# Optimization experiments

Measured on AMD Instinct MI355X. Metric: run time of the kernel, lower is better.

The kernel has to match this reference:

```python
import jax, jax.numpy as jnp
import numpy as np

N = 100000
E = 3200000
IN_F = 256
OUT_F = 64
ALPHA = 0.2  # LeakyReLU negative slope


def setup_inputs() -> dict:
    key = jax.random.key(0)
    k1, k2, k3, k4 = jax.random.split(key, 4)
    adj = jax.random.randint(k1, (2, E), 0, N, dtype=jnp.int64)
    x = jax.random.normal(k2, (N, IN_F), dtype=jnp.float32)
    # xavier-normal-ish scales
    W_fc = jax.random.normal(k3, (OUT_F, IN_F), dtype=jnp.float32) * (1.414 * np.sqrt(2.0 / (IN_F + OUT_F)))
    b_fc = jnp.zeros((OUT_F,), dtype=jnp.float32)
    a = jax.random.normal(k4, (1, 2 * OUT_F), dtype=jnp.float32) * (1.414 * np.sqrt(2.0 / (1 + 2 * OUT_F)))
    return {"adj": adj, "x": x, "W_fc": W_fc, "b_fc": b_fc, "a": a}


def reference(adj, x, W_fc, b_fc, a):
    src = adj[0]  # [E]
    dst = adj[1]  # [E]
    h = x @ W_fc.T + b_fc                       # [N, OUT_F]
    a1, a2 = a[0, :OUT_F], a[0, OUT_F:]         # split of attention vector
    # e = leakyrelu(a . [h_src || h_dst]) computed without materializing concat
    s1 = h @ a1                                  # [N]
    s2 = h @ a2                                  # [N]
    e = s1[src] + s2[dst]                        # [E]
    e = jnp.where(e > 0, e, ALPHA * e)           # LeakyReLU
    # dgl edge_softmax: softmax over edges grouped by destination node
    m = jax.ops.segment_max(e, dst, num_segments=N)     # [N]
    ex = jnp.exp(e - m[dst])                             # [E]
    denom = jax.ops.segment_sum(ex, dst, num_segments=N) # [N]
    att = ex / denom[dst]                                # [E]
    # SparseTensor(row=src, col=dst, value=att) @ h -> out[src] += att * h[dst]
    h_prime = jax.ops.segment_sum(att[:, None] * h[dst], src, num_segments=N)  # [N, OUT_F]
    return jax.nn.elu(h_prime)  # concat=True branch
```

## Files before the change

kernel.cpp:

```cpp
#include <hip/hip_runtime.h>
#include <math.h>

#define N_NODES 100000
#define N_EDGES 3200000
#define IN_F 256
#define OUT_F 64
#define LRELU_ALPHA 0.2f
#define NBKT 782
#define CAP 4480

typedef unsigned short u16;
typedef __attribute__((ext_vector_type(8))) short short8;
typedef __attribute__((ext_vector_type(4))) float floatx4;

__device__ inline u16 f2bf(float f) {
  unsigned u = __float_as_uint(f);
  u += 0x7FFFu + ((u >> 16) & 1u);
  return (u16)(u >> 16);
}
__device__ inline float bf2f(u16 h) {
  return __uint_as_float(((unsigned)h) << 16);
}

__global__ __launch_bounds__(256) void k_prep(const float* __restrict__ W,
                                              u16* __restrict__ Wbf,
                                              int* __restrict__ sfill,
                                              int* __restrict__ dfill) {
  if (blockIdx.x < 64) {
    int i = blockIdx.x * 256 + threadIdx.x;
    Wbf[i] = f2bf(W[i]);
  } else {
    for (int i = threadIdx.x; i < NBKT; i += 256) {
      sfill[i] = 0;
      dfill[i] = 0;
    }
  }
}

__global__ __launch_bounds__(256) void k_linear(
    const float* __restrict__ x, const u16* __restrict__ Wbf,
    const float* __restrict__ b, const float* __restrict__ a,
    u16* __restrict__ hbf, float* __restrict__ s1, float* __restrict__ s2) {
  __shared__ u16 Wlds[64 * 264];

  const int t = threadIdx.x;
#pragma unroll
  for (int p = 0; p < 8; p++) {
    int c = p * 256 + t;
    int row = c >> 5;
    int kc = (c & 31) * 8;
    *(short8*)&Wlds[row * 264 + kc] = *(const short8*)&Wbf[row * 256 + kc];
  }
  __syncthreads();

  const int w = t >> 6;
  const int lane = t & 63;
  const int col = lane & 15;
  const int q = lane >> 4;
  const int m0 = blockIdx.x * 64 + w * 16;

  floatx4 acc[4];
#pragma unroll
  for (int nt = 0; nt < 4; nt++) acc[nt] = (floatx4){0.f, 0.f, 0.f, 0.f};

  int mrow = m0 + col;
  if (mrow > N_NODES - 1) mrow = N_NODES - 1;
  const float* xrow = x + (size_t)mrow * IN_F + q * 8;

#pragma unroll
  for (int kk = 0; kk < 8; kk++) {
    float4 f0 = *(const float4*)(xrow + kk * 32);
    float4 f1 = *(const float4*)(xrow + kk * 32 + 4);
    short8 af;
    af[0] = (short)f2bf(f0.x);
    af[1] = (short)f2bf(f0.y);
    af[2] = (short)f2bf(f0.z);
    af[3] = (short)f2bf(f0.w);
    af[4] = (short)f2bf(f1.x);
    af[5] = (short)f2bf(f1.y);
    af[6] = (short)f2bf(f1.z);
    af[7] = (short)f2bf(f1.w);
#pragma unroll
    for (int nt = 0; nt < 4; nt++) {
      short8 bfr = *(const short8*)&Wlds[(nt * 16 + col) * 264 + kk * 32 + q * 8];
      acc[nt] = __builtin_amdgcn_mfma_f32_16x16x32_bf16(af, bfr, acc[nt], 0, 0, 0);
    }
  }

  float bv[4], a1v[4], a2v[4];
#pragma unroll
  for (int nt = 0; nt < 4; nt++) {
    bv[nt] = b[nt * 16 + col];
    a1v[nt] = a[nt * 16 + col];
    a2v[nt] = a[OUT_F + nt * 16 + col];
  }
#pragma unroll
  for (int r = 0; r < 4; r++) {
    int node = m0 + q * 4 + r;
    float p1 = 0.f, p2 = 0.f;
#pragma unroll
    for (int nt = 0; nt < 4; nt++) {
      float hv = acc[nt][r] + bv[nt];
      if (node < N_NODES) hbf[(size_t)node * OUT_F + nt * 16 + col] = f2bf(hv);
      p1 = fmaf(hv, a1v[nt], p1);
      p2 = fmaf(hv, a2v[nt], p2);
    }
#pragma unroll
    for (int s = 1; s < 16; s <<= 1) {
      p1 += __shfl_xor(p1, s, 16);
      p2 += __shfl_xor(p2, s, 16);
    }
    if (col == 0 && node < N_NODES) {
      s1[node] = p1;
      s2[node] = p2;
    }
  }
}

#define PBT 512
#define EPT_P 8
#define PEB (PBT * EPT_P)
__global__ __launch_bounds__(PBT) void k_place(
    const int* __restrict__ src, const int* __restrict__ dst,
    const float* __restrict__ s1, const float* __restrict__ s2,
    int* __restrict__ sfill, int* __restrict__ dfill,
    float2* __restrict__ pairS, float2* __restrict__ pairD) {
  __shared__ int lc[NBKT];
  __shared__ int ofs[NBKT];
  __shared__ int gbase[NBKT];
  __shared__ int tot;
  __shared__ float2 stage[PEB];
  __shared__ u16 stageB[PEB];

  const int t = threadIdx.x;
  const int base = blockIdx.x * PEB + t;

  float ex[EPT_P];
  int pk[EPT_P];
  int bs[EPT_P];

  for (int i = t; i < NBKT; i += PBT) lc[i] = 0;
  if (t == 0) tot = 0;
  __syncthreads();

#pragma unroll
  for (int j = 0; j < EPT_P; j++) {
    int e = base + j * PBT;
    if (e < N_EDGES) {
      int s = src[e];
      int d = dst[e];
      float v = s1[s] + s2[d];
      v = v > 0.f ? v : LRELU_ALPHA * v;
      ex[j] = __expf(v);
      pk[j] = d | ((s & 127) << 17);
      bs[j] = s >> 7;
      atomicAdd(&lc[bs[j]], 1);
    } else {
      bs[j] = -1;
    }
  }
  __syncthreads();

  for (int i = t; i < NBKT; i += PBT) {
    int c = lc[i];
    if (c) {
      gbase[i] = i * CAP + atomicAdd(&sfill[i], c);
      ofs[i] = atomicAdd(&tot, c);
    }
  }
  __syncthreads();
  const int nval = tot;
  for (int i = t; i < NBKT; i += PBT) lc[i] = 0;
  __syncthreads();

#pragma unroll
  for (int j = 0; j < EPT_P; j++) {
    if (bs[j] >= 0) {
      int r = atomicAdd(&lc[bs[j]], 1);
      int idx = ofs[bs[j]] + r;
      stage[idx] = make_float2(ex[j], __int_as_float(pk[j]));
      stageB[idx] = (u16)bs[j];
    }
  }
  __syncthreads();

  for (int i = t; i < nval; i += PBT) {
    int bkt = stageB[i];
    pairS[gbase[bkt] + (i - ofs[bkt])] = stage[i];
  }
  __syncthreads();

  for (int i = t; i < NBKT; i += PBT) lc[i] = 0;
  if (t == 0) tot = 0;
  __syncthreads();
#pragma unroll
  for (int j = 0; j < EPT_P; j++) {
    if (bs[j] >= 0) {
      int bd = (pk[j] & 0x1FFFF) >> 7;
      atomicAdd(&lc[bd], 1);
    }
  }
  __syncthreads();

  for (int i = t; i < NBKT; i += PBT) {
    int c = lc[i];
    if (c) {
      gbase[i] = i * CAP + atomicAdd(&dfill[i], c);
      ofs[i] = atomicAdd(&tot, c);
    }
  }
  __syncthreads();
  for (int i = t; i < NBKT; i += PBT) lc[i] = 0;
  __syncthreads();

#pragma unroll
  for (int j = 0; j < EPT_P; j++) {
    if (bs[j] >= 0) {
      int d = pk[j] & 0x1FFFF;
      int bd = d >> 7;
      int r = atomicAdd(&lc[bd], 1);
      int idx = ofs[bd] + r;
      stage[idx] = make_float2(ex[j], __int_as_float(d & 127));
      stageB[idx] = (u16)bd;
    }
  }
  __syncthreads();

  for (int i = t; i < nval; i += PBT) {
    int bkt = stageB[i];
    pairD[gbase[bkt] + (i - ofs[bkt])] = stage[i];
  }
}

__global__ __launch_bounds__(256) void k_denom(const int* __restrict__ dfill,
                                               const float2* __restrict__ pairD,
                                               float* __restrict__ denom_r) {
  __shared__ float lacc[128];
  const int t = threadIdx.x;
  const int bkt = blockIdx.x;
  if (t < 128) lacc[t] = 0.f;
  __syncthreads();
  int beg = bkt * CAP;
  int end = beg + dfill[bkt];
  for (int i = beg + t; i < end; i += 256) {
    float2 p = pairD[i];
    atomicAdd(&lacc[__float_as_int(p.y)], p.x);
  }
  __syncthreads();
  if (t < 128) {
    int node = bkt * 128 + t;
    if (node < N_NODES) denom_r[node] = 1.0f / lacc[t];
  }
}

__global__ __launch_bounds__(256) void k_sort2(
    const int* __restrict__ sfill, const float2* __restrict__ pairS,
    const float* __restrict__ denom_r, float2* __restrict__ pairA,
    int2* __restrict__ rowbe) {
  __shared__ int lcnt[128];
  __shared__ int cursor[128];
  __shared__ int w0tot;
  const int t = threadIdx.x;
  const int bkt = blockIdx.x;
  if (t < 128) lcnt[t] = 0;
  __syncthreads();

  const int beg = bkt * CAP;
  const int end = beg + sfill[bkt];

  for (int i = beg + t; i < end; i += 256) {
    int pkv = __float_as_int(pairS[i].y);
    atomicAdd(&lcnt[(pkv >> 17) & 127], 1);
  }
  __syncthreads();

  const int lane = t & 63;
  int v = (t < 128) ? lcnt[t] : 0;
  int val = v;
#pragma unroll
  for (int ofs = 1; ofs < 64; ofs <<= 1) {
    int u = __shfl_up(val, ofs, 64);
    if (lane >= ofs) val += u;
  }
  if (t == 63) w0tot = val;
  __syncthreads();
  int excl = val - v + ((t >= 64 && t < 128) ? w0tot : 0);
  if (t < 128) {
    cursor[t] = beg + excl;
    int node = bkt * 128 + t;
    if (node < N_NODES) rowbe[node] = make_int2(beg + excl, beg + excl + v);
  }
  __syncthreads();

  for (int i = beg + t; i < end; i += 256) {
    float2 p = pairS[i];
    int pkv = __float_as_int(p.y);
    int sl = (pkv >> 17) & 127;
    int d = pkv & 0x1FFFF;
    float att = p.x * denom_r[d];
    int pos = atomicAdd(&cursor[sl], 1);
    pairA[pos] = make_float2(att, __int_as_float(d));
  }
}

__global__ __launch_bounds__(256) void k_aggregate(
    const int2* __restrict__ rowbe, const float2* __restrict__ pairA,
    const u16* __restrict__ hbf, float* __restrict__ out) {
  int wid = (blockIdx.x * 256 + threadIdx.x) >> 6;
  int lane = threadIdx.x & 63;
  int g = lane >> 4;
  int sl = lane & 15;
  int node = wid * 4 + g;
  int2 be = (node < N_NODES) ? rowbe[node] : make_int2(0, 0);
  float4 acc = make_float4(0.f, 0.f, 0.f, 0.f);
  int i = be.x;
  const int end = be.y;
  for (; i + 1 < end; i += 2) {
    float2 p0 = pairA[i];
    float2 p1 = pairA[i + 1];
    int d0 = __float_as_int(p0.y);
    int d1 = __float_as_int(p1.y);
    ushort4 q0 = *(const ushort4*)&hbf[(size_t)d0 * OUT_F + sl * 4];
    ushort4 q1 = *(const ushort4*)&hbf[(size_t)d1 * OUT_F + sl * 4];
    acc.x = fmaf(p0.x, bf2f(q0.x), acc.x);
    acc.y = fmaf(p0.x, bf2f(q0.y), acc.y);
    acc.z = fmaf(p0.x, bf2f(q0.z), acc.z);
    acc.w = fmaf(p0.x, bf2f(q0.w), acc.w);
    acc.x = fmaf(p1.x, bf2f(q1.x), acc.x);
    acc.y = fmaf(p1.x, bf2f(q1.y), acc.y);
    acc.z = fmaf(p1.x, bf2f(q1.z), acc.z);
    acc.w = fmaf(p1.x, bf2f(q1.w), acc.w);
  }
  if (i < end) {
    float2 p = pairA[i];
    int d = __float_as_int(p.y);
    ushort4 q = *(const ushort4*)&hbf[(size_t)d * OUT_F + sl * 4];
    acc.x = fmaf(p.x, bf2f(q.x), acc.x);
    acc.y = fmaf(p.x, bf2f(q.y), acc.y);
    acc.z = fmaf(p.x, bf2f(q.z), acc.z);
    acc.w = fmaf(p.x, bf2f(q.w), acc.w);
  }
  if (node < N_NODES) {
    float4 o;
    o.x = acc.x > 0.f ? acc.x : expm1f(acc.x);
    o.y = acc.y > 0.f ? acc.y : expm1f(acc.y);
    o.z = acc.z > 0.f ? acc.z : expm1f(acc.z);
    o.w = acc.w > 0.f ? acc.w : expm1f(acc.w);
    *(float4*)(out + (size_t)node * OUT_F + sl * 4) = o;
  }
}

extern "C" void kernel_launch(void* const* d_in, const int* in_sizes, int n_in,
                              void* d_out, int out_size, void* d_ws,
                              size_t ws_size, hipStream_t stream) {
  const int* adj = (const int*)d_in[0];
  const float* x = (const float*)d_in[1];
  const float* W = (const float*)d_in[2];
  const float* b = (const float*)d_in[3];
  const float* a = (const float*)d_in[4];
  float* out = (float*)d_out;

  float* ws = (float*)d_ws;
  float* s1v = ws;
  float* s2v = ws + 100000;
  float* denom_r = ws + 200000;
  int* sfill = (int*)(ws + 300000);
  int* dfill = (int*)(ws + 300800);
  int2* rowbe = (int2*)(ws + 301600);
  float2* pairS = (float2*)(ws + 501600);
  float2* pairD = (float2*)(ws + 7508320);
  u16* hbf = (u16*)(ws + 14515040);
  u16* Wbf = (u16*)(ws + 17715040);

  float2* pairA = pairD;

  const int* src = adj;
  const int* dst = adj + N_EDGES;

  k_prep<<<65, 256, 0, stream>>>(W, Wbf, sfill, dfill);
  k_linear<<<(N_NODES + 63) / 64, 256, 0, stream>>>(x, Wbf, b, a, hbf, s1v, s2v);
  k_place<<<(N_EDGES + PEB - 1) / PEB, PBT, 0, stream>>>(
      src, dst, s1v, s2v, sfill, dfill, pairS, pairD);
  k_denom<<<NBKT, 256, 0, stream>>>(dfill, pairD, denom_r);
  k_sort2<<<NBKT, 256, 0, stream>>>(sfill, pairS, denom_r, pairA, rowbe);
  k_aggregate<<<(N_NODES + 15) / 16, 256, 0, stream>>>(rowbe, pairA, hbf, out);
}
```

Baseline: 409.9 us.

## Fuse per-bucket sort and aggregation into one kernel using LDS staging

Merges the source-bucket counting sort and the SpMM aggregation into a single kernel. Each 512-thread block sorts its bucket's edges into a shared-memory staging array instead of writing pairA and rowbe to global memory. It then aggregates h rows for its 128 nodes directly from that array. This removes a global write and read of about 25MB plus one launch. In exchange it uses about 36KB of LDS per block, which limits occupancy, and gives only 782 blocks, so the gather phase runs with less parallelism than the previous 6250-block aggregate kernel.

```diff
diff --git a/kernel.cpp b/kernel.cpp
--- a/kernel.cpp
+++ b/kernel.cpp
@@ -253,23 +253,28 @@
   }
 }
 
-__global__ __launch_bounds__(256) void k_sort2(
+#define SAT 512
+__global__ __launch_bounds__(SAT) void k_sortagg(
     const int* __restrict__ sfill, const float2* __restrict__ pairS,
-    const float* __restrict__ denom_r, float2* __restrict__ pairA,
-    int2* __restrict__ rowbe) {
+    const float* __restrict__ denom_r, const u16* __restrict__ hbf,
+    float* __restrict__ out) {
+  __shared__ float2 stg[CAP];
   __shared__ int lcnt[128];
-  __shared__ int cursor[128];
+  __shared__ int cur[128];
+  __shared__ int nbeg[128];
+  __shared__ int nend[128];
   __shared__ int w0tot;
   const int t = threadIdx.x;
   const int bkt = blockIdx.x;
+
   if (t < 128) lcnt[t] = 0;
   __syncthreads();
 
-  const int beg = bkt * CAP;
-  const int end = beg + sfill[bkt];
-
-  for (int i = beg + t; i < end; i += 256) {
-    int pkv = __float_as_int(pairS[i].y);
+  const int gbeg = bkt * CAP;
+  const int ne = sfill[bkt];
+
+  for (int i = t; i < ne; i += SAT) {
+    int pkv = __float_as_int(pairS[gbeg + i].y);
     atomicAdd(&lcnt[(pkv >> 17) & 127], 1);
   }
   __syncthreads();
@@ -278,75 +283,71 @@
   int v = (t < 128) ? lcnt[t] : 0;
   int val = v;
 #pragma unroll
-  for (int ofs = 1; ofs < 64; ofs <<= 1) {
-    int u = __shfl_up(val, ofs, 64);
-    if (lane >= ofs) val += u;
+  for (int o = 1; o < 64; o <<= 1) {
+    int u = __shfl_up(val, o, 64);
+    if (lane >= o) val += u;
   }
   if (t == 63) w0tot = val;
   __syncthreads();
-  int excl = val - v + ((t >= 64 && t < 128) ? w0tot : 0);
   if (t < 128) {
-    cursor[t] = beg + excl;
-    int node = bkt * 128 + t;
-    if (node < N_NODES) rowbe[node] = make_int2(beg + excl, beg + excl + v);
-  }
-  __syncthreads();
-
-  for (int i = beg + t; i < end; i += 256) {
-    float2 p = pairS[i];
+    int excl = val - v + ((t >= 64) ? w0tot : 0);
+    cur[t] = excl;
+    nbeg[t] = excl;
+    nend[t] = excl + v;
+  }
+  __syncthreads();
+
+  for (int i = t; i < ne; i += SAT) {
+    float2 p = pairS[gbeg + i];
     int pkv = __float_as_int(p.y);
     int sl = (pkv >> 17) & 127;
     int d = pkv & 0x1FFFF;
     float att = p.x * denom_r[d];
-    int pos = atomicAdd(&cursor[sl], 1);
-    pairA[pos] = make_float2(att, __int_as_float(d));
-  }
-}
-
-__global__ __launch_bounds__(256) void k_aggregate(
-    const int2* __restrict__ rowbe, const float2* __restrict__ pairA,
-    const u16* __restrict__ hbf, float* __restrict__ out) {
-  int wid = (blockIdx.x * 256 + threadIdx.x) >> 6;
-  int lane = threadIdx.x & 63;
-  int g = lane >> 4;
-  int sl = lane & 15;
-  int node = wid * 4 + g;
-  int2 be = (node < N_NODES) ? rowbe[node] : make_int2(0, 0);
-  float4 acc = make_float4(0.f, 0.f, 0.f, 0.f);
-  int i = be.x;
-  const int end = be.y;
-  for (; i + 1 < end; i += 2) {
-    float2 p0 = pairA[i];
-    float2 p1 = pairA[i + 1];
-    int d0 = __float_as_int(p0.y);
-    int d1 = __float_as_int(p1.y);
-    ushort4 q0 = *(const ushort4*)&hbf[(size_t)d0 * OUT_F + sl * 4];
-    ushort4 q1 = *(const ushort4*)&hbf[(size_t)d1 * OUT_F + sl * 4];
-    acc.x = fmaf(p0.x, bf2f(q0.x), acc.x);
-    acc.y = fmaf(p0.x, bf2f(q0.y), acc.y);
-    acc.z = fmaf(p0.x, bf2f(q0.z), acc.z);
-    acc.w = fmaf(p0.x, bf2f(q0.w), acc.w);
-    acc.x = fmaf(p1.x, bf2f(q1.x), acc.x);
-    acc.y = fmaf(p1.x, bf2f(q1.y), acc.y);
-    acc.z = fmaf(p1.x, bf2f(q1.z), acc.z);
-    acc.w = fmaf(p1.x, bf2f(q1.w), acc.w);
-  }
-  if (i < end) {
-    float2 p = pairA[i];
-    int d = __float_as_int(p.y);
-    ushort4 q = *(const ushort4*)&hbf[(size_t)d * OUT_F + sl * 4];
-    acc.x = fmaf(p.x, bf2f(q.x), acc.x);
-    acc.y = fmaf(p.x, bf2f(q.y), acc.y);
-    acc.z = fmaf(p.x, bf2f(q.z), acc.z);
-    acc.w = fmaf(p.x, bf2f(q.w), acc.w);
-  }
-  if (node < N_NODES) {
-    float4 o;
-    o.x = acc.x > 0.f ? acc.x : expm1f(acc.x);
-    o.y = acc.y > 0.f ? acc.y : expm1f(acc.y);
-    o.z = acc.z > 0.f ? acc.z : expm1f(acc.z);
-    o.w = acc.w > 0.f ? acc.w : expm1f(acc.w);
-    *(float4*)(out + (size_t)node * OUT_F + sl * 4) = o;
+    int pos = atomicAdd(&cur[sl], 1);
+    stg[pos] = make_float2(att, __int_as_float(d));
+  }
+  __syncthreads();
+
+  const int G = t >> 4;
+  const int sl = t & 15;
+  for (int nl = G; nl < 128; nl += 32) {
+    int node = bkt * 128 + nl;
+    int i = nbeg[nl];
+    const int e0 = nend[nl];
+    float4 acc = make_float4(0.f, 0.f, 0.f, 0.f);
+    for (; i + 1 < e0; i += 2) {
+      float2 p0 = stg[i];
+      float2 p1 = stg[i + 1];
+      int d0 = __float_as_int(p0.y);
+      int d1 = __float_as_int(p1.y);
+      ushort4 q0 = *(const ushort4*)&hbf[(size_t)d0 * OUT_F + sl * 4];
+      ushort4 q1 = *(const ushort4*)&hbf[(size_t)d1 * OUT_F + sl * 4];
+      acc.x = fmaf(p0.x, bf2f(q0.x), acc.x);
+      acc.y = fmaf(p0.x, bf2f(q0.y), acc.y);
+      acc.z = fmaf(p0.x, bf2f(q0.z), acc.z);
+      acc.w = fmaf(p0.x, bf2f(q0.w), acc.w);
+      acc.x = fmaf(p1.x, bf2f(q1.x), acc.x);
+      acc.y = fmaf(p1.x, bf2f(q1.y), acc.y);
+      acc.z = fmaf(p1.x, bf2f(q1.z), acc.z);
+      acc.w = fmaf(p1.x, bf2f(q1.w), acc.w);
+    }
+    if (i < e0) {
+      float2 p = stg[i];
+      int d = __float_as_int(p.y);
+      ushort4 q = *(const ushort4*)&hbf[(size_t)d * OUT_F + sl * 4];
+      acc.x = fmaf(p.x, bf2f(q.x), acc.x);
+      acc.y = fmaf(p.x, bf2f(q.y), acc.y);
+      acc.z = fmaf(p.x, bf2f(q.z), acc.z);
+      acc.w = fmaf(p.x, bf2f(q.w), acc.w);
+    }
+    if (node < N_NODES) {
+      float4 o;
+      o.x = acc.x > 0.f ? acc.x : expm1f(acc.x);
+      o.y = acc.y > 0.f ? acc.y : expm1f(acc.y);
+      o.z = acc.z > 0.f ? acc.z : expm1f(acc.z);
+      o.w = acc.w > 0.f ? acc.w : expm1f(acc.w);
+      *(float4*)(out + (size_t)node * OUT_F + sl * 4) = o;
+    }
   }
 }
 
@@ -366,13 +367,10 @@
   float* denom_r = ws + 200000;
   int* sfill = (int*)(ws + 300000);
   int* dfill = (int*)(ws + 300800);
-  int2* rowbe = (int2*)(ws + 301600);
-  float2* pairS = (float2*)(ws + 501600);
-  float2* pairD = (float2*)(ws + 7508320);
-  u16* hbf = (u16*)(ws + 14515040);
-  u16* Wbf = (u16*)(ws + 17715040);
-
-  float2* pairA = pairD;
+  float2* pairS = (float2*)(ws + 301600);
+  float2* pairD = (float2*)(ws + 7308320);
+  u16* hbf = (u16*)(ws + 14315040);
+  u16* Wbf = (u16*)(ws + 17515040);
 
   const int* src = adj;
   const int* dst = adj + N_EDGES;
@@ -382,6 +380,5 @@
   k_place<<<(N_EDGES + PEB - 1) / PEB, PBT, 0, stream>>>(
       src, dst, s1v, s2v, sfill, dfill, pairS, pairD);
   k_denom<<<NBKT, 256, 0, stream>>>(dfill, pairD, denom_r);
-  k_sort2<<<NBKT, 256, 0, stream>>>(sfill, pairS, denom_r, pairA, rowbe);
-  k_aggregate<<<(N_NODES + 15) / 16, 256, 0, stream>>>(rowbe, pairA, hbf, out);
-}
+  k_sortagg<<<NBKT, SAT, 0, stream>>>(sfill, pairS, denom_r, hbf, out);
+}
```

Result: faster. 369.9 us (-9.8%).
